# Optimization experiments

Hardware: AMD Instinct MI355X
Metric: run time of the kernel (lower is better)

Reference implementation:

```python
import jax, jax.numpy as jnp
import numpy as np

H, Wd, Z = 480, 480, 2
BN_EPS = 1e-3  # PointPillars-style BatchNorm1d(eps=1e-3)


def setup_inputs() -> dict:
    key = jax.random.key(0)
    ks = jax.random.split(key, 5)
    bs, seq, N, Cin, C = 2, 1, 20000, 4, 64
    features = jax.random.normal(ks[0], (bs, seq, N, Cin), dtype=jnp.float32)
    cx = jax.random.randint(ks[1], (bs, seq, N), 0, H)
    cy = jax.random.randint(ks[2], (bs, seq, N), 0, Wd)
    cz = jax.random.randint(ks[3], (bs, seq, N), 0, Z)
    coords = jnp.stack([cx, cy, cz], axis=-1).astype(jnp.int64)
    W = jax.random.normal(ks[4], (C, Cin), dtype=jnp.float32) * 0.1
    gamma = jnp.ones((C,), jnp.float32)
    beta = jnp.zeros((C,), jnp.float32)
    running_mean = jnp.zeros((C,), jnp.float32)
    running_var = jnp.ones((C,), jnp.float32)
    return {"features": features, "coords": coords, "W": W, "gamma": gamma,
            "beta": beta, "running_mean": running_mean, "running_var": running_var}


def reference(features, coords, W, gamma, beta, running_mean, running_var):
    bs, seq, N, Cin = features.shape
    feats = features.reshape(bs * seq, N, Cin)          # [B, N, 4]
    co = coords.reshape(bs * seq, N, 3)
    # flattened voxel index: x*W*Z + y*Z + z, in [0, H*W*Z)
    idx = co[:, :, 0] * (Wd * Z) + co[:, :, 1] * Z + co[:, :, 2]  # [B, N]
    # linear (no bias) + BatchNorm1d (inference stats) + ReLU
    x = jnp.einsum('bnc,uc->bnu', feats, W)             # [B, N, 64]
    x = (x - running_mean) * (gamma / jnp.sqrt(running_var + BN_EPS)) + beta
    x = jax.nn.relu(x)
    B, n, c = x.shape
    # scatter-max into a zero-initialized dense grid (matches torch scatter reduce='max' into zeros)
    x_max = jnp.zeros((B, H * Wd * Z, c), x.dtype)
    x_max = x_max.at[jnp.arange(B)[:, None], idx].max(x)  # [B, HWZ, C]
    # [B, HWZ, C] -> [B, C, H, W, Z] -> [B, Z, C, H, W] -> [B, Z*C, H, W]
    x_max = jnp.transpose(x_max, (0, 2, 1)).reshape(B, c, H, Wd, Z)
    x_max = jnp.transpose(x_max, (0, 4, 1, 2, 3)).reshape(B, Z * c, H, Wd)
    x_perm = jnp.transpose(x, (0, 2, 1))                # [B, C, N]
    return x_perm, jnp.squeeze(x_max)
```

## Files before the change

kernel.cpp:

```cpp
#include <hip/hip_runtime.h>

#define HH  480
#define WW  480
#define ZZ  2
#define CC  64
#define CIN 4
#define BN_EPS 1e-3f
#define ROWS  (2 * ZZ * HH)
#define MAXR  256
#define CTB   16
#define TPAD  484

__global__ __launch_bounds__(256) void pfn_clear_cnt(int* __restrict__ rowcnt)
{
    int i = blockIdx.x * blockDim.x + threadIdx.x;
    if (i < ROWS) rowcnt[i] = 0;
}

__global__ __launch_bounds__(256) void pfn_pass_a(
    const float* __restrict__ feats,
    const int*   __restrict__ coords,
    const float* __restrict__ W,
    const float* __restrict__ gamma,
    const float* __restrict__ beta,
    const float* __restrict__ rmean,
    const float* __restrict__ rvar,
    float*  __restrict__ out0,
    float4* __restrict__ rowf4,
    int*    __restrict__ roww,
    int*    __restrict__ rowcnt,
    int N, int B)
{
    int pt = blockIdx.x * blockDim.x + threadIdx.x;
    if (pt >= B * N) return;
    int n = pt % N;
    int b = pt / N;
    const int c0 = blockIdx.y * 8;

    float4 f = *reinterpret_cast<const float4*>(feats + (long)pt * CIN);

    #pragma unroll
    for (int k = 0; k < 8; ++k) {
        int c = c0 + k;
        float scale = gamma[c] * rsqrtf(rvar[c] + BN_EPS);
        float bias  = beta[c] - rmean[c] * scale;
        float v = f.x * W[c*4+0] + f.y * W[c*4+1] + f.z * W[c*4+2] + f.w * W[c*4+3];
        v = fmaxf(v * scale + bias, 0.0f);
        out0[((long)(b * CC + c)) * N + n] = v;
    }

    if (blockIdx.y == 0) {
        int cx = coords[(long)pt*3 + 0];
        int cy = coords[(long)pt*3 + 1];
        int cz = coords[(long)pt*3 + 2];
        int row = (b * ZZ + cz) * HH + cx;
        int k = atomicAdd(&rowcnt[row], 1);
        if (k < MAXR) {
            rowf4[(long)row * MAXR + k] = f;
            roww [(long)row * MAXR + k] = cy;
        }
    }
}

__global__ __launch_bounds__(256) void pfn_pass_b(
    const float4* __restrict__ rowf4,
    const int*    __restrict__ roww,
    const int*    __restrict__ rowcnt,
    const float*  __restrict__ W,
    const float*  __restrict__ gamma,
    const float*  __restrict__ beta,
    const float*  __restrict__ rmean,
    const float*  __restrict__ rvar,
    float* __restrict__ out1)
{
    int bid  = blockIdx.x;
    int q    = bid / ROWS;
    int row  = bid - q * ROWS;
    int h = row % HH;
    int z = (row / HH) % ZZ;
    int b = row / (HH * ZZ);
    const int c0 = q * CTB;
    const int tid = threadIdx.x;

    __shared__ float tile[CTB][TPAD];
    __shared__ float lw[4][CTB], lsc[CTB], lbi[CTB];

    float4* t4 = reinterpret_cast<float4*>(&tile[0][0]);
    #pragma unroll
    for (int r = 0; r < 8; ++r) {
        int i = tid + r * 256;
        if (i < CTB * TPAD / 4) t4[i] = make_float4(0.f, 0.f, 0.f, 0.f);
    }
    if (tid < CTB) {
        int c = c0 + tid;
        float s = gamma[c] * rsqrtf(rvar[c] + BN_EPS);
        lsc[tid] = s;
        lbi[tid] = beta[c] - rmean[c] * s;
        lw[0][tid] = W[c*4+0]; lw[1][tid] = W[c*4+1];
        lw[2][tid] = W[c*4+2]; lw[3][tid] = W[c*4+3];
    }
    __syncthreads();

    int cnt = rowcnt[row];
    cnt = cnt < MAXR ? cnt : MAXR;
    const long rb = (long)row * MAXR;

    for (int i = tid; i < cnt * CTB; i += 256) {
        int j  = i >> 4;
        int cc = i & (CTB - 1);
        float4 f = rowf4[rb + j];
        int    w = roww [rb + j];
        float v = f.x*lw[0][cc] + f.y*lw[1][cc] + f.z*lw[2][cc] + f.w*lw[3][cc];
        v = fmaxf(v * lsc[cc] + lbi[cc], 0.0f);
        atomicMax(reinterpret_cast<unsigned int*>(&tile[cc][w]), __float_as_uint(v));
    }
    __syncthreads();

    const int c2 = tid >> 7;
    const int w4 = tid & 127;
    const long plane = (long)HH * WW;
    const long base  = (((long)((b * ZZ + z) * CC + c0)) * HH + h) * WW;
    if (w4 < 120) {
        #pragma unroll
        for (int r = 0; r < 8; ++r) {
            int c = c2 + r * 2;
            *reinterpret_cast<float4*>(out1 + base + (long)c * plane + (long)w4 * 4)
                = *reinterpret_cast<const float4*>(&tile[c][w4 * 4]);
        }
    }
}

__global__ __launch_bounds__(256) void pfn_fallback(
    const float* __restrict__ feats, const int* __restrict__ coords,
    const float* __restrict__ W, const float* __restrict__ gamma,
    const float* __restrict__ beta, const float* __restrict__ rmean,
    const float* __restrict__ rvar, float* __restrict__ out0,
    float* __restrict__ out1, int N, int B)
{
    long gid = (long)blockIdx.x * blockDim.x + threadIdx.x;
    long total = (long)CC * B * N;
    if (gid >= total) return;
    int n = (int)(gid % N); int rem = (int)(gid / N);
    int b = rem % B; int c = rem / B;
    long pt = (long)b * N + n;
    float4 f = *reinterpret_cast<const float4*>(feats + pt * CIN);
    float scale = gamma[c] * rsqrtf(rvar[c] + BN_EPS);
    float bias  = beta[c] - rmean[c] * scale;
    float val = f.x*W[c*4] + f.y*W[c*4+1] + f.z*W[c*4+2] + f.w*W[c*4+3];
    val = fmaxf(val * scale + bias, 0.0f);
    out0[((long)(b * CC + c)) * N + n] = val;
    int cx = coords[pt*3+0], cy = coords[pt*3+1], cz = coords[pt*3+2];
    long o1 = ((((long)(b * ZZ + cz)) * CC + c) * HH + cx) * WW + cy;
    atomicMax(reinterpret_cast<unsigned int*>(out1) + o1, __float_as_uint(val));
}

extern "C" void kernel_launch(void* const* d_in, const int* in_sizes, int n_in,
                              void* d_out, int out_size, void* d_ws, size_t ws_size,
                              hipStream_t stream) {
    const float* feats  = (const float*)d_in[0];
    const int*   coords = (const int*)d_in[1];
    const float* W      = (const float*)d_in[2];
    const float* gamma  = (const float*)d_in[3];
    const float* beta   = (const float*)d_in[4];
    const float* rmean  = (const float*)d_in[5];
    const float* rvar   = (const float*)d_in[6];

    const int B = 2;
    const int N = in_sizes[0] / (B * CIN);

    float* out0 = (float*)d_out;
    long   out0_sz = (long)B * CC * N;
    float* out1 = out0 + out0_sz;

    const size_t rowf4_bytes = (size_t)ROWS * MAXR * sizeof(float4);
    const size_t roww_bytes  = (size_t)ROWS * MAXR * sizeof(int);
    const size_t cnt_bytes   = (size_t)ROWS * sizeof(int);
    const size_t need = rowf4_bytes + roww_bytes + cnt_bytes;

    if (ws_size >= need) {
        float4* rowf4  = (float4*)d_ws;
        int*    roww   = (int*)((char*)d_ws + rowf4_bytes);
        int*    rowcnt = (int*)((char*)d_ws + rowf4_bytes + roww_bytes);

        pfn_clear_cnt<<<(ROWS + 255) / 256, 256, 0, stream>>>(rowcnt);

        dim3 gridA((B * N + 255) / 256, 8);
        pfn_pass_a<<<gridA, 256, 0, stream>>>(
            feats, coords, W, gamma, beta, rmean, rvar, out0,
            rowf4, roww, rowcnt, N, B);

        int blocksB = ROWS * (CC / CTB);
        pfn_pass_b<<<blocksB, 256, 0, stream>>>(
            rowf4, roww, rowcnt, W, gamma, beta, rmean, rvar, out1);
    } else {
        size_t out1_bytes = (size_t)B * ZZ * CC * HH * WW * sizeof(float);
        (void)hipMemsetAsync(out1, 0, out1_bytes, stream);
        long total = (long)CC * B * N;
        pfn_fallback<<<(int)((total + 255) / 256), 256, 0, stream>>>(
            feats, coords, W, gamma, beta, rmean, rvar, out0, out1, N, B);
    }
}
```

Baseline: 51.84 us.

## Retile scatter-max pass by channel and row chunk for contiguous output writes

The second pass now gives each block one channel and a chunk of 16 consecutive H rows, instead of one row and 16 channels. A shared prefix sum and row map flatten the points of those rows into a single work list. Each block then writes one fully contiguous 16x480 slab of the output plane. The aim is better write coalescing and fewer per-block setup loads. In exchange, each point is re-read once per channel (64 times instead of 4), and a serial prefix and row-map build is added.

```diff
diff --git a/kernel.cpp b/kernel.cpp
--- a/kernel.cpp
+++ b/kernel.cpp
@@ -6,10 +6,10 @@
 #define CC  64
 #define CIN 4
 #define BN_EPS 1e-3f
-#define ROWS  (2 * ZZ * HH)
-#define MAXR  256
-#define CTB   16
-#define TPAD  484
+#define ROWS   (2 * ZZ * HH)
+#define MAXR   256
+#define HCHUNK 16
+#define TPAD   484
 
 __global__ __launch_bounds__(256) void pfn_clear_cnt(int* __restrict__ rowcnt)
 {
@@ -73,59 +73,67 @@
     const float*  __restrict__ rvar,
     float* __restrict__ out1)
 {
-    int bid  = blockIdx.x;
-    int q    = bid / ROWS;
-    int row  = bid - q * ROWS;
-    int h = row % HH;
-    int z = (row / HH) % ZZ;
-    int b = row / (HH * ZZ);
-    const int c0 = q * CTB;
+    const int bid = blockIdx.x;
+    const int hc  = bid % 30;
+    const int cl  = bid / 30;
+    const int c   = cl & 63;
+    const int bz  = cl >> 6;
+    const int row0 = bz * HH + hc * HCHUNK;
     const int tid = threadIdx.x;
 
-    __shared__ float tile[CTB][TPAD];
-    __shared__ float lw[4][CTB], lsc[CTB], lbi[CTB];
+    __shared__ float tile[HCHUNK][TPAD];
+    __shared__ int scnt[HCHUNK], pref[HCHUNK + 1];
+    __shared__ unsigned char rowmap[HCHUNK * MAXR];
 
     float4* t4 = reinterpret_cast<float4*>(&tile[0][0]);
     #pragma unroll
     for (int r = 0; r < 8; ++r) {
         int i = tid + r * 256;
-        if (i < CTB * TPAD / 4) t4[i] = make_float4(0.f, 0.f, 0.f, 0.f);
-    }
-    if (tid < CTB) {
-        int c = c0 + tid;
-        float s = gamma[c] * rsqrtf(rvar[c] + BN_EPS);
-        lsc[tid] = s;
-        lbi[tid] = beta[c] - rmean[c] * s;
-        lw[0][tid] = W[c*4+0]; lw[1][tid] = W[c*4+1];
-        lw[2][tid] = W[c*4+2]; lw[3][tid] = W[c*4+3];
-    }
-    __syncthreads();
-
-    int cnt = rowcnt[row];
-    cnt = cnt < MAXR ? cnt : MAXR;
-    const long rb = (long)row * MAXR;
-
-    for (int i = tid; i < cnt * CTB; i += 256) {
-        int j  = i >> 4;
-        int cc = i & (CTB - 1);
-        float4 f = rowf4[rb + j];
-        int    w = roww [rb + j];
-        float v = f.x*lw[0][cc] + f.y*lw[1][cc] + f.z*lw[2][cc] + f.w*lw[3][cc];
-        v = fmaxf(v * lsc[cc] + lbi[cc], 0.0f);
-        atomicMax(reinterpret_cast<unsigned int*>(&tile[cc][w]), __float_as_uint(v));
-    }
-    __syncthreads();
-
-    const int c2 = tid >> 7;
-    const int w4 = tid & 127;
-    const long plane = (long)HH * WW;
-    const long base  = (((long)((b * ZZ + z) * CC + c0)) * HH + h) * WW;
-    if (w4 < 120) {
+        if (i < HCHUNK * TPAD / 4) t4[i] = make_float4(0.f, 0.f, 0.f, 0.f);
+    }
+    if (tid < HCHUNK) {
+        int cn = rowcnt[row0 + tid];
+        scnt[tid] = cn < MAXR ? cn : MAXR;
+    }
+    __syncthreads();
+    if (tid == 0) {
+        int acc = 0;
         #pragma unroll
-        for (int r = 0; r < 8; ++r) {
-            int c = c2 + r * 2;
-            *reinterpret_cast<float4*>(out1 + base + (long)c * plane + (long)w4 * 4)
-                = *reinterpret_cast<const float4*>(&tile[c][w4 * 4]);
+        for (int r = 0; r < HCHUNK; ++r) { pref[r] = acc; acc += scnt[r]; }
+        pref[HCHUNK] = acc;
+    }
+    __syncthreads();
+    if (tid < HCHUNK) {
+        int p0 = pref[tid], cn = scnt[tid];
+        for (int j = 0; j < cn; ++j) rowmap[p0 + j] = (unsigned char)tid;
+    }
+    __syncthreads();
+
+    const float w0 = W[c*4+0], w1 = W[c*4+1], w2 = W[c*4+2], w3 = W[c*4+3];
+    const float sc = gamma[c] * rsqrtf(rvar[c] + BN_EPS);
+    const float bi = beta[c] - rmean[c] * sc;
+
+    const int T = pref[HCHUNK];
+    for (int i = tid; i < T; i += 256) {
+        int r  = rowmap[i];
+        int jj = i - pref[r];
+        long rb = (long)(row0 + r) * MAXR + jj;
+        float4 f = rowf4[rb];
+        int    w = roww [rb];
+        float v = f.x*w0 + f.y*w1 + f.z*w2 + f.w*w3;
+        v = fmaxf(v * sc + bi, 0.0f);
+        atomicMax(reinterpret_cast<unsigned int*>(&tile[r][w]), __float_as_uint(v));
+    }
+    __syncthreads();
+
+    float4* out_f4 = reinterpret_cast<float4*>(out1) + (long)bid * (HCHUNK * WW / 4);
+    #pragma unroll
+    for (int rr = 0; rr < 8; ++rr) {
+        int g = tid + rr * 256;
+        if (g < HCHUNK * WW / 4) {
+            int hl = g / 120;
+            int w4 = g - hl * 120;
+            out_f4[g] = *reinterpret_cast<const float4*>(&tile[hl][w4 * 4]);
         }
     }
 }
@@ -189,7 +197,7 @@
             feats, coords, W, gamma, beta, rmean, rvar, out0,
             rowf4, roww, rowcnt, N, B);
 
-        int blocksB = ROWS * (CC / CTB);
+        int blocksB = 2 * ZZ * CC * (HH / HCHUNK);
         pfn_pass_b<<<blocksB, 256, 0, stream>>>(
             rowf4, roww, rowcnt, W, gamma, beta, rmean, rvar, out1);
     } else {
```

After: 53.71 us. +3.6%, slower.

## Restructure scatter pass to process 32 channels per block with double-buffered tiles

Applied to the files above, without the earlier changes.

Pass B now launches two blocks per row, each covering 32 channels in four 8-channel chunks. Each thread loads one point into registers once and reuses it across all chunks. Two shared tiles alternate so that zeroing and scattering the next chunk can overlap with the stores of the current one. This cuts the number of blocks and repeated point loads, but adds syncs per chunk and loads the BN parameters per thread from global memory.

```diff
diff --git a/kernel.cpp b/kernel.cpp
--- a/kernel.cpp
+++ b/kernel.cpp
@@ -8,7 +8,7 @@
 #define BN_EPS 1e-3f
 #define ROWS  (2 * ZZ * HH)
 #define MAXR  256
-#define CTB   16
+#define CTB   8
 #define TPAD  484
 
 __global__ __launch_bounds__(256) void pfn_clear_cnt(int* __restrict__ rowcnt)
@@ -73,60 +73,92 @@
     const float*  __restrict__ rvar,
     float* __restrict__ out1)
 {
-    int bid  = blockIdx.x;
-    int q    = bid / ROWS;
-    int row  = bid - q * ROWS;
-    int h = row % HH;
-    int z = (row / HH) % ZZ;
-    int b = row / (HH * ZZ);
-    const int c0 = q * CTB;
+    const int bid = blockIdx.x;
+    const int row = bid >> 1;
+    const int cq  = (bid & 1) * 4;
+    const int h  = row % HH;
+    const int z  = (row / HH) % ZZ;
+    const int b  = row / (HH * ZZ);
     const int tid = threadIdx.x;
 
-    __shared__ float tile[CTB][TPAD];
-    __shared__ float lw[4][CTB], lsc[CTB], lbi[CTB];
-
-    float4* t4 = reinterpret_cast<float4*>(&tile[0][0]);
-    #pragma unroll
-    for (int r = 0; r < 8; ++r) {
-        int i = tid + r * 256;
-        if (i < CTB * TPAD / 4) t4[i] = make_float4(0.f, 0.f, 0.f, 0.f);
-    }
-    if (tid < CTB) {
-        int c = c0 + tid;
-        float s = gamma[c] * rsqrtf(rvar[c] + BN_EPS);
-        lsc[tid] = s;
-        lbi[tid] = beta[c] - rmean[c] * s;
-        lw[0][tid] = W[c*4+0]; lw[1][tid] = W[c*4+1];
-        lw[2][tid] = W[c*4+2]; lw[3][tid] = W[c*4+3];
-    }
-    __syncthreads();
+    __shared__ float tile[2][CTB * TPAD];
 
     int cnt = rowcnt[row];
     cnt = cnt < MAXR ? cnt : MAXR;
-    const long rb = (long)row * MAXR;
-
-    for (int i = tid; i < cnt * CTB; i += 256) {
-        int j  = i >> 4;
-        int cc = i & (CTB - 1);
-        float4 f = rowf4[rb + j];
-        int    w = roww [rb + j];
-        float v = f.x*lw[0][cc] + f.y*lw[1][cc] + f.z*lw[2][cc] + f.w*lw[3][cc];
-        v = fmaxf(v * lsc[cc] + lbi[cc], 0.0f);
-        atomicMax(reinterpret_cast<unsigned int*>(&tile[cc][w]), __float_as_uint(v));
+    float4 pf = make_float4(0.f, 0.f, 0.f, 0.f);
+    int    pw = 0;
+    if (tid < cnt) {
+        pf = rowf4[(long)row * MAXR + tid];
+        pw = roww [(long)row * MAXR + tid];
+    }
+
+    {
+        float4* t4 = reinterpret_cast<float4*>(tile[0]);
+        #pragma unroll
+        for (int r = 0; r < 4; ++r) {
+            int i = tid + r * 256;
+            if (i < CTB * TPAD / 4) t4[i] = make_float4(0.f, 0.f, 0.f, 0.f);
+        }
     }
     __syncthreads();
 
-    const int c2 = tid >> 7;
-    const int w4 = tid & 127;
+    if (tid < cnt) {
+        #pragma unroll
+        for (int j = 0; j < 8; ++j) {
+            int c = (cq + 0) * 8 + j;
+            float sc = gamma[c] * rsqrtf(rvar[c] + BN_EPS);
+            float bi = beta[c] - rmean[c] * sc;
+            float v = pf.x*W[c*4+0] + pf.y*W[c*4+1] + pf.z*W[c*4+2] + pf.w*W[c*4+3];
+            v = fmaxf(v * sc + bi, 0.0f);
+            atomicMax(reinterpret_cast<unsigned int*>(&tile[0][j * TPAD + pw]),
+                      __float_as_uint(v));
+        }
+    }
+    __syncthreads();
+
     const long plane = (long)HH * WW;
-    const long base  = (((long)((b * ZZ + z) * CC + c0)) * HH + h) * WW;
-    if (w4 < 120) {
-        #pragma unroll
-        for (int r = 0; r < 8; ++r) {
-            int c = c2 + r * 2;
-            *reinterpret_cast<float4*>(out1 + base + (long)c * plane + (long)w4 * 4)
-                = *reinterpret_cast<const float4*>(&tile[c][w4 * 4]);
-        }
+    const int  ch = tid >> 5;
+    const int  wl = tid & 31;
+    int buf = 0;
+
+    #pragma unroll
+    for (int k = 0; k < 4; ++k) {
+        {
+            const long obase =
+                (((long)((b * ZZ + z) * CC + (cq + k) * 8 + ch)) * HH + h) * WW;
+            #pragma unroll
+            for (int r = 0; r < 4; ++r) {
+                int w4 = wl + r * 32;
+                if (w4 < 120) {
+                    *reinterpret_cast<float4*>(out1 + obase + (long)w4 * 4)
+                        = *reinterpret_cast<const float4*>(&tile[buf][ch * TPAD + w4 * 4]);
+                }
+            }
+        }
+        if (k < 3) {
+            float4* t4 = reinterpret_cast<float4*>(tile[buf ^ 1]);
+            #pragma unroll
+            for (int r = 0; r < 4; ++r) {
+                int i = tid + r * 256;
+                if (i < CTB * TPAD / 4) t4[i] = make_float4(0.f, 0.f, 0.f, 0.f);
+            }
+            __syncthreads();
+            if (tid < cnt) {
+                #pragma unroll
+                for (int j = 0; j < 8; ++j) {
+                    int c = (cq + k + 1) * 8 + j;
+                    float sc = gamma[c] * rsqrtf(rvar[c] + BN_EPS);
+                    float bi = beta[c] - rmean[c] * sc;
+                    float v = pf.x*W[c*4+0] + pf.y*W[c*4+1] + pf.z*W[c*4+2] + pf.w*W[c*4+3];
+                    v = fmaxf(v * sc + bi, 0.0f);
+                    atomicMax(reinterpret_cast<unsigned int*>(
+                                  &tile[buf ^ 1][j * TPAD + pw]),
+                              __float_as_uint(v));
+                }
+            }
+            __syncthreads();
+        }
+        buf ^= 1;
     }
 }
 
@@ -189,7 +221,7 @@
             feats, coords, W, gamma, beta, rmean, rvar, out0,
             rowf4, roww, rowcnt, N, B);
 
-        int blocksB = ROWS * (CC / CTB);
+        int blocksB = ROWS * 2;
         pfn_pass_b<<<blocksB, 256, 0, stream>>>(
             rowf4, roww, rowcnt, W, gamma, beta, rmean, rvar, out1);
     } else {
```

New measurement: 51.82 us. No clear change (-0.0%).
